# Kernel tuning notes

Hardware: AMD Instinct MI355X
Metric: run time of the kernel (lower is better)

Reference implementation:

```python
import jax, jax.numpy as jnp
import numpy as np

HDIM = 64

def setup_inputs() -> dict:
    key = jax.random.key(0)
    ks = jax.random.split(key, 5)
    B, T, D = 4, 2048, 1024
    x = jax.random.normal(ks[0], (B, T, D), dtype=jnp.float32)
    s = 1.0 / np.sqrt(D)
    W_qkv = jax.random.normal(ks[1], (D, 3 * D), dtype=jnp.float32) * s
    b_qkv = jax.random.normal(ks[2], (3 * D,), dtype=jnp.float32) * 0.02
    W_out = jax.random.normal(ks[3], (D, D), dtype=jnp.float32) * s
    b_out = jax.random.normal(ks[4], (D,), dtype=jnp.float32) * 0.02
    return {"x": x, "W_qkv": W_qkv, "b_qkv": b_qkv, "W_out": W_out, "b_out": b_out}

def reference(x, W_qkv, b_qkv, W_out, b_out):
    B, T, D = x.shape
    H = D // HDIM
    qkv = x @ W_qkv + b_qkv                          # [B,T,3D]
    q, k, v = jnp.split(qkv, 3, axis=-1)
    # [B,T,D] -> [B,H,T,Hdim]
    q = q.reshape(B, T, H, HDIM).transpose(0, 2, 1, 3)
    k = k.reshape(B, T, H, HDIM).transpose(0, 2, 1, 3)
    v = v.reshape(B, T, H, HDIM).transpose(0, 2, 1, 3)
    scores = jnp.einsum('bhqd,bhkd->bhqk', q, k) / jnp.sqrt(jnp.float32(HDIM))
    causal = jnp.tril(jnp.ones((T, T), dtype=bool))
    scores = jnp.where(causal[None, None], scores, -jnp.inf)
    weights = jax.nn.softmax(scores, axis=-1)        # dropout_prob=0 -> identity
    out = jnp.einsum('bhqk,bhkd->bhqd', weights, v)  # [B,H,T,Hdim]
    out = out.transpose(0, 2, 1, 3).reshape(B, T, D)
    return out @ W_out + b_out
```

## Files before the change

kernel.cpp:

```cpp
#include <hip/hip_runtime.h>

typedef __attribute__((ext_vector_type(8))) short short8;
typedef __attribute__((ext_vector_type(4))) short s16x4;
typedef __attribute__((ext_vector_type(4))) float f32x4;

#define AS1 __attribute__((address_space(1)))
#define AS3 __attribute__((address_space(3)))

__device__ __forceinline__ void gload_lds16(const void* g, void* l) {
  __builtin_amdgcn_global_load_lds((const AS1 void*)g, (AS3 void*)l, 16, 0, 0);
}

__device__ __forceinline__ unsigned short f2bf(float f) {
  unsigned int u = __float_as_uint(f);
  u += 0x7fffu + ((u >> 16) & 1u);
  return (unsigned short)(u >> 16);
}

__global__ __launch_bounds__(256) void k_convert(const float* __restrict__ in,
                                                 unsigned short* __restrict__ out) {
  long i = (long)blockIdx.x * 256 + threadIdx.x;
  const float4* p = (const float4*)in + i * 2;
  float4 a = p[0], b = p[1];
  short8 o;
  o[0] = (short)f2bf(a.x); o[1] = (short)f2bf(a.y);
  o[2] = (short)f2bf(a.z); o[3] = (short)f2bf(a.w);
  o[4] = (short)f2bf(b.x); o[5] = (short)f2bf(b.y);
  o[6] = (short)f2bf(b.z); o[7] = (short)f2bf(b.w);
  ((short8*)out)[i] = o;
}

__global__ __launch_bounds__(256) void k_transpose_w(const float* __restrict__ w,
                                                     unsigned short* __restrict__ wt,
                                                     int K, int N) {
  __shared__ float t[64][65];
  const int tilesN = N >> 6;
  const int tk = blockIdx.x / tilesN, tn = blockIdx.x % tilesN;
  const int c = threadIdx.x & 63, r0 = (threadIdx.x >> 6) * 16;
#pragma unroll
  for (int i = 0; i < 16; ++i)
    t[r0 + i][c] = w[(long)(tk * 64 + r0 + i) * N + tn * 64 + c];
  __syncthreads();
#pragma unroll
  for (int i = 0; i < 16; ++i)
    wt[(long)(tn * 64 + r0 + i) * K + tk * 64 + c] = f2bf(t[c][r0 + i]);
}

__global__ __launch_bounds__(256) void k_transpose_v(const unsigned short* __restrict__ qkv,
                                                     unsigned short* __restrict__ vt) {
  __shared__ __align__(16) unsigned short t[64][72];
  const int tt = blockIdx.x & 31, bh = blockIdx.x >> 5;
  const int b = bh >> 4, h = bh & 15;
  const int r = threadIdx.x >> 2, c0 = (threadIdx.x & 3) * 16;
  const unsigned short* src = qkv + (long)(b * 2048 + tt * 64 + r) * 3072 + 2048 + h * 64 + c0;
  *(short8*)&t[r][c0] = *(const short8*)src;
  *(short8*)&t[r][c0 + 8] = *(const short8*)(src + 8);
  __syncthreads();
  short8 w0, w1;
#pragma unroll
  for (int i = 0; i < 8; ++i) w0[i] = (short)t[c0 + i][r];
#pragma unroll
  for (int i = 0; i < 8; ++i) w1[i] = (short)t[c0 + 8 + i][r];
  unsigned short* dst = vt + (long)(bh * 64 + r) * 2048 + tt * 64 + c0;
  *(short8*)dst = w0;
  *(short8*)(dst + 8) = w1;
}

template <int OUT_BF16>
__global__ __launch_bounds__(256) void k_gemm(const unsigned short* __restrict__ A,
                                              const unsigned short* __restrict__ BT,
                                              const float* __restrict__ bias,
                                              void* __restrict__ out,
                                              int M, int N, int K) {
  __shared__ __align__(16) unsigned short As[2][128 * 64];
  __shared__ __align__(16) unsigned short Bs[2][128 * 64];
  const int tid = threadIdx.x, lane = tid & 63, wid = tid >> 6;
  const int r16 = lane & 15, khi = lane >> 4;
  const int wr = wid >> 1, wc = wid & 1;
  const int tilesN = N >> 7;
  const int cpx = gridDim.x >> 3;
  const int bid = ((int)blockIdx.x & 7) * cpx + ((int)blockIdx.x >> 3);
  const int tm = bid / tilesN, tn = bid % tilesN;
  const long m0 = (long)tm * 128, n0 = (long)tn * 128;
  f32x4 acc[4][4] = {};
  const int srow = tid >> 3;
  const int scol = ((tid & 7) ^ (srow & 7)) * 8;
  const unsigned short* aSrc = A + (m0 + srow) * K + scol;
  const unsigned short* bSrc = BT + (n0 + srow) * K + scol;
  unsigned short* aDst = &As[0][0] + tid * 8;
  unsigned short* bDst = &Bs[0][0] + tid * 8;
  const int nk = K >> 6;

#pragma unroll
  for (int call = 0; call < 4; ++call) {
    gload_lds16(aSrc + (long)call * 32 * K, aDst + call * 2048);
    gload_lds16(bSrc + (long)call * 32 * K, bDst + call * 2048);
  }

  int cur = 0;
  for (int ki = 0; ki < nk; ++ki) {
    __builtin_amdgcn_s_barrier();
    if (ki + 1 < nk) {
      const long k0 = (long)(ki + 1) * 64;
#pragma unroll
      for (int call = 0; call < 4; ++call) {
        gload_lds16(aSrc + (long)call * 32 * K + k0, aDst + (cur ^ 1) * 8192 + call * 2048);
        gload_lds16(bSrc + (long)call * 32 * K + k0, bDst + (cur ^ 1) * 8192 + call * 2048);
      }
      asm volatile("s_waitcnt vmcnt(8)" ::: "memory");
    } else {
      asm volatile("s_waitcnt vmcnt(0)" ::: "memory");
    }
    __builtin_amdgcn_s_barrier();
    __builtin_amdgcn_s_setprio(1);
#pragma unroll
    for (int kk = 0; kk < 2; ++kk) {
      const int pc = ((kk * 4 + khi) ^ (r16 & 7)) * 8;
      short8 af[4], bf[4];
#pragma unroll
      for (int m = 0; m < 4; ++m)
        af[m] = *(const short8*)&As[cur][(wr * 64 + m * 16 + r16) * 64 + pc];
#pragma unroll
      for (int n = 0; n < 4; ++n)
        bf[n] = *(const short8*)&Bs[cur][(wc * 64 + n * 16 + r16) * 64 + pc];
#pragma unroll
      for (int m = 0; m < 4; ++m)
#pragma unroll
        for (int n = 0; n < 4; ++n)
          acc[m][n] = __builtin_amdgcn_mfma_f32_16x16x32_bf16(af[m], bf[n], acc[m][n], 0, 0, 0);
    }
    __builtin_amdgcn_s_setprio(0);
    cur ^= 1;
  }
#pragma unroll
  for (int m = 0; m < 4; ++m) {
    long row = m0 + wr * 64 + m * 16 + khi * 4;
#pragma unroll
    for (int n = 0; n < 4; ++n) {
      int col = (int)n0 + wc * 64 + n * 16 + r16;
      float bv = bias[col];
#pragma unroll
      for (int j = 0; j < 4; ++j) {
        float v = acc[m][n][j] + bv;
        if (OUT_BF16)
          ((unsigned short*)out)[(row + j) * N + col] = f2bf(v);
        else
          ((float*)out)[(row + j) * N + col] = v;
      }
    }
  }
}

__global__ __launch_bounds__(512) void k_attn(const unsigned short* __restrict__ qkv,
                                              const unsigned short* __restrict__ vt,
                                              unsigned short* __restrict__ aout) {
  __shared__ __align__(16) unsigned short Ks[2][64 * 64];
  __shared__ __align__(16) unsigned short VTs[2][64 * 64];
  __shared__ __align__(16) unsigned short Ps[8][16 * 72];
  const int tid = threadIdx.x, lane = tid & 63, wid = tid >> 6;
  const int r16 = lane & 15, khi = lane >> 4;
  const int qt = 15 - (int)(blockIdx.x >> 6), bh = blockIdx.x & 63;
  const int b = bh >> 4, h = bh & 15;
  const long qrow0 = (long)b * 2048 + qt * 128;

  const int srow = wid * 8 + (lane >> 3);
  const int lck = (lane & 7) ^ (srow & 7);
  const unsigned short* kbase =
      qkv + ((long)b * 2048 + srow) * 3072 + 1024 + h * 64 + lck * 8;
  const unsigned short* vbase = vt + ((long)bh * 64 + srow) * 2048 + lck * 8;

  const long qrow = qrow0 + wid * 16 + r16;
  const short8 qf0 = *(const short8*)&qkv[qrow * 3072 + h * 64 + khi * 8];
  const short8 qf1 = *(const short8*)&qkv[qrow * 3072 + h * 64 + 32 + khi * 8];

  gload_lds16(kbase, &Ks[0][wid * 512]);
  gload_lds16(vbase, &VTs[0][wid * 512]);

  const int ktmax = 2 * qt + 1;
  const int ktw = (qt * 128 + wid * 16 + 15) >> 6;
  const int qg = qt * 128 + wid * 16 + r16;
  const float SC = 0.18033688f;
  float m_run = -1e30f, l_run = 0.f;
  f32x4 o[4] = {};

  for (int kt = 0; kt <= ktmax; ++kt) {
    const int cur = kt & 1;
    __builtin_amdgcn_s_barrier();
    if (kt < ktmax) {
      gload_lds16(kbase + (long)(kt + 1) * 64 * 3072, &Ks[cur ^ 1][wid * 512]);
      gload_lds16(vbase + (kt + 1) * 64, &VTs[cur ^ 1][wid * 512]);
      asm volatile("s_waitcnt vmcnt(2)" ::: "memory");
    } else {
      asm volatile("s_waitcnt vmcnt(0)" ::: "memory");
    }
    __builtin_amdgcn_s_barrier();
    if (kt > ktw) continue;

    f32x4 s[4] = {};
    __builtin_amdgcn_s_setprio(1);
#pragma unroll
    for (int kk = 0; kk < 2; ++kk) {
      const int pc = ((kk * 4 + khi) ^ (r16 & 7)) * 8;
      const short8 qf = kk ? qf1 : qf0;
#pragma unroll
      for (int n = 0; n < 4; ++n) {
        short8 kf = *(const short8*)&Ks[cur][(n * 16 + r16) * 64 + pc];
        s[n] = __builtin_amdgcn_mfma_f32_16x16x32_bf16(kf, qf, s[n], 0, 0, 0);
      }
    }
    __builtin_amdgcn_s_setprio(0);

    const bool need_mask = (kt * 64 + 63) > (qt * 128 + wid * 16);
    if (need_mask) {
      const int ktB = kt * 64;
#pragma unroll
      for (int n = 0; n < 4; ++n)
#pragma unroll
        for (int j = 0; j < 4; ++j)
          if ((ktB + n * 16 + khi * 4 + j) > qg) s[n][j] = -1e30f;
    }

    float pmn[4];
#pragma unroll
    for (int n = 0; n < 4; ++n)
      pmn[n] = fmaxf(fmaxf(s[n][0], s[n][1]), fmaxf(s[n][2], s[n][3]));
    float pm = fmaxf(fmaxf(pmn[0], pmn[1]), fmaxf(pmn[2], pmn[3]));
    pm = fmaxf(pm, __shfl_xor(pm, 16, 64));
    pm = fmaxf(pm, __shfl_xor(pm, 32, 64));
    const float pmS = pm * SC;
    const float mn = fmaxf(m_run, pmS);
    if (!__all(pmS <= m_run)) {
      const float alpha = __builtin_amdgcn_exp2f(m_run - mn);
      l_run *= alpha;
#pragma unroll
      for (int n = 0; n < 4; ++n)
#pragma unroll
        for (int j = 0; j < 4; ++j) o[n][j] *= alpha;
    }
    m_run = mn;

    const float nmn = -mn;
    float rsum = 0.f;
    unsigned int pk[8];
#pragma unroll
    for (int n = 0; n < 4; ++n) {
      float e0 = __builtin_amdgcn_exp2f(fmaf(s[n][0], SC, nmn));
      float e1 = __builtin_amdgcn_exp2f(fmaf(s[n][1], SC, nmn));
      float e2 = __builtin_amdgcn_exp2f(fmaf(s[n][2], SC, nmn));
      float e3 = __builtin_amdgcn_exp2f(fmaf(s[n][3], SC, nmn));
      rsum += (e0 + e1) + (e2 + e3);
      pk[n * 2] = __builtin_amdgcn_perm(__float_as_uint(e1), __float_as_uint(e0), 0x07060302u);
      pk[n * 2 + 1] = __builtin_amdgcn_perm(__float_as_uint(e3), __float_as_uint(e2), 0x07060302u);
    }
    rsum += __shfl_xor(rsum, 16, 64);
    rsum += __shfl_xor(rsum, 32, 64);
    l_run += rsum;

#pragma unroll
    for (int n = 0; n < 4; ++n) {
      uint2 pw = {pk[n * 2], pk[n * 2 + 1]};
      *(uint2*)&Ps[wid][r16 * 72 + n * 16 + khi * 4] = pw;
    }

    __builtin_amdgcn_s_setprio(1);
#pragma unroll
    for (int kk = 0; kk < 2; ++kk) {
      const short8 pf = *(const short8*)&Ps[wid][r16 * 72 + kk * 32 + khi * 8];
      const int pc = ((kk * 4 + khi) ^ (r16 & 7)) * 8;
#pragma unroll
      for (int n = 0; n < 4; ++n) {
        short8 vf = *(const short8*)&VTs[cur][(n * 16 + r16) * 64 + pc];
        o[n] = __builtin_amdgcn_mfma_f32_16x16x32_bf16(vf, pf, o[n], 0, 0, 0);
      }
    }
    __builtin_amdgcn_s_setprio(0);
  }

  const float inv = 1.f / l_run;
#pragma unroll
  for (int n = 0; n < 4; ++n) {
    s16x4 ow;
#pragma unroll
    for (int j = 0; j < 4; ++j) ow[j] = (short)f2bf(o[n][j] * inv);
    *(s16x4*)&aout[qrow * 1024 + h * 64 + n * 16 + khi * 4] = ow;
  }
}

extern "C" void kernel_launch(void* const* d_in, const int* in_sizes, int n_in,
                              void* d_out, int out_size, void* d_ws, size_t ws_size,
                              hipStream_t stream) {
  (void)in_sizes; (void)n_in; (void)out_size; (void)ws_size;
  const float* x = (const float*)d_in[0];
  const float* Wqkv = (const float*)d_in[1];
  const float* bqkv = (const float*)d_in[2];
  const float* Wout = (const float*)d_in[3];
  const float* bout = (const float*)d_in[4];
  char* ws = (char*)d_ws;
  unsigned short* xb    = (unsigned short*)(ws + 0);
  unsigned short* wqkvt = (unsigned short*)(ws + (16l << 20));
  unsigned short* woutt = (unsigned short*)(ws + (22l << 20));
  unsigned short* qkv   = (unsigned short*)(ws + (24l << 20));
  unsigned short* vt    = (unsigned short*)(ws + (72l << 20));
  unsigned short* aout  = xb;

  k_convert<<<4096, 256, 0, stream>>>(x, xb);
  k_transpose_w<<<768, 256, 0, stream>>>(Wqkv, wqkvt, 1024, 3072);
  k_transpose_w<<<256, 256, 0, stream>>>(Wout, woutt, 1024, 1024);
  k_gemm<1><<<64 * 24, 256, 0, stream>>>(xb, wqkvt, bqkv, qkv, 8192, 3072, 1024);
  k_transpose_v<<<2048, 256, 0, stream>>>(qkv, vt);
  k_attn<<<16 * 64, 512, 0, stream>>>(qkv, vt, aout);
  k_gemm<0><<<64 * 8, 256, 0, stream>>>(aout, woutt, bout, d_out, 8192, 1024, 1024);
}
```

Before: 247.9 us.

## Use 256x128 GEMM tiles with 8 waves and a 3-stage interleaved LDS pipeline

Grows the GEMM block tile to 256x128 with 512 threads and adds a triple-buffered LDS ring, prefetching two K-steps ahead. Global-to-LDS loads are split into chunks and interleaved between MFMA sub-phases, separated by barriers. The aim is better reuse of B tiles and more overlap of memory latency with MFMA work. In exchange it uses more LDS (144KB), adds extra barriers per K-step, and launches fewer blocks (256 for the output projection), which may leave CUs underused.

```diff
diff --git a/kernel.cpp b/kernel.cpp
--- a/kernel.cpp
+++ b/kernel.cpp
@@ -67,77 +67,107 @@
 }
 
 template <int OUT_BF16>
-__global__ __launch_bounds__(256) void k_gemm(const unsigned short* __restrict__ A,
+__global__ __launch_bounds__(512) void k_gemm(const unsigned short* __restrict__ A,
                                               const unsigned short* __restrict__ BT,
                                               const float* __restrict__ bias,
                                               void* __restrict__ out,
                                               int M, int N, int K) {
-  __shared__ __align__(16) unsigned short As[2][128 * 64];
-  __shared__ __align__(16) unsigned short Bs[2][128 * 64];
+  __shared__ __align__(16) unsigned short As[3][256 * 64];
+  __shared__ __align__(16) unsigned short Bs[3][128 * 64];
   const int tid = threadIdx.x, lane = tid & 63, wid = tid >> 6;
   const int r16 = lane & 15, khi = lane >> 4;
-  const int wr = wid >> 1, wc = wid & 1;
+  const int wm = wid >> 1, wn = wid & 1;
   const int tilesN = N >> 7;
   const int cpx = gridDim.x >> 3;
   const int bid = ((int)blockIdx.x & 7) * cpx + ((int)blockIdx.x >> 3);
   const int tm = bid / tilesN, tn = bid % tilesN;
-  const long m0 = (long)tm * 128, n0 = (long)tn * 128;
+  const long m0 = (long)tm * 256, n0 = (long)tn * 128;
   f32x4 acc[4][4] = {};
-  const int srow = tid >> 3;
-  const int scol = ((tid & 7) ^ (srow & 7)) * 8;
-  const unsigned short* aSrc = A + (m0 + srow) * K + scol;
-  const unsigned short* bSrc = BT + (n0 + srow) * K + scol;
-  unsigned short* aDst = &As[0][0] + tid * 8;
-  unsigned short* bDst = &Bs[0][0] + tid * 8;
+  const int lr8 = lane >> 3;
+  const int scol = ((lane & 7) ^ lr8) * 8;
+  const unsigned short* aSrc = A + (m0 + wid * 32 + lr8) * K + scol;
+  const unsigned short* bSrc = BT + (n0 + wid * 16 + lr8) * K + scol;
   const int nk = K >> 6;
-
-#pragma unroll
-  for (int call = 0; call < 4; ++call) {
-    gload_lds16(aSrc + (long)call * 32 * K, aDst + call * 2048);
-    gload_lds16(bSrc + (long)call * 32 * K, bDst + call * 2048);
+  const int pc0 = (khi ^ (r16 & 7)) * 8;
+  const int pc1 = ((4 + khi) ^ (r16 & 7)) * 8;
+
+#define SA(buf, kt, c) gload_lds16(aSrc + (long)(kt) * 64 + (c) * 8 * K, &As[buf][wid * 2048 + (c) * 512])
+#define SB(buf, kt, c) gload_lds16(bSrc + (long)(kt) * 64 + (c) * 8 * K, &Bs[buf][wid * 1024 + (c) * 512])
+#define AF(m, pc) (*(const short8*)&Ab[(wm * 64 + (m) * 16 + r16) * 64 + (pc)])
+#define BF(n, pc) (*(const short8*)&Bb[(wn * 64 + (n) * 16 + r16) * 64 + (pc)])
+
+  SA(0, 0, 0); SA(0, 0, 1); SA(0, 0, 2); SA(0, 0, 3); SB(0, 0, 0); SB(0, 0, 1);
+  if (nk > 1) { SA(1, 1, 0); SA(1, 1, 1); SA(1, 1, 2); SA(1, 1, 3); SB(1, 1, 0); SB(1, 1, 1); }
+
+  int ct = 0;
+  for (int t = 0; t < nk; ++t) {
+    const int st = (ct + 2 >= 3) ? ct - 1 : ct + 2;
+    if (t + 1 < nk) asm volatile("s_waitcnt vmcnt(6)" ::: "memory");
+    else            asm volatile("s_waitcnt vmcnt(0)" ::: "memory");
+    __builtin_amdgcn_s_barrier();
+    const bool stg = (t + 2) < nk;
+    const unsigned short* Ab = As[ct];
+    const unsigned short* Bb = Bs[ct];
+    short8 bf[4], af[2];
+
+    if (stg) { SA(st, t + 2, 0); SA(st, t + 2, 1); }
+    bf[0] = BF(0, pc0); bf[1] = BF(1, pc0); bf[2] = BF(2, pc0); bf[3] = BF(3, pc0);
+    af[0] = AF(0, pc0); af[1] = AF(1, pc0);
+    __builtin_amdgcn_s_setprio(1);
+#pragma unroll
+    for (int n = 0; n < 4; ++n) {
+      acc[0][n] = __builtin_amdgcn_mfma_f32_16x16x32_bf16(af[0], bf[n], acc[0][n], 0, 0, 0);
+      acc[1][n] = __builtin_amdgcn_mfma_f32_16x16x32_bf16(af[1], bf[n], acc[1][n], 0, 0, 0);
+    }
+    __builtin_amdgcn_s_setprio(0);
+    __builtin_amdgcn_s_barrier();
+
+    if (stg) { SA(st, t + 2, 2); SA(st, t + 2, 3); }
+    af[0] = AF(2, pc0); af[1] = AF(3, pc0);
+    __builtin_amdgcn_s_setprio(1);
+#pragma unroll
+    for (int n = 0; n < 4; ++n) {
+      acc[2][n] = __builtin_amdgcn_mfma_f32_16x16x32_bf16(af[0], bf[n], acc[2][n], 0, 0, 0);
+      acc[3][n] = __builtin_amdgcn_mfma_f32_16x16x32_bf16(af[1], bf[n], acc[3][n], 0, 0, 0);
+    }
+    __builtin_amdgcn_s_setprio(0);
+    __builtin_amdgcn_s_barrier();
+
+    if (stg) { SB(st, t + 2, 0); SB(st, t + 2, 1); }
+    bf[0] = BF(0, pc1); bf[1] = BF(1, pc1); bf[2] = BF(2, pc1); bf[3] = BF(3, pc1);
+    af[0] = AF(0, pc1); af[1] = AF(1, pc1);
+    __builtin_amdgcn_s_setprio(1);
+#pragma unroll
+    for (int n = 0; n < 4; ++n) {
+      acc[0][n] = __builtin_amdgcn_mfma_f32_16x16x32_bf16(af[0], bf[n], acc[0][n], 0, 0, 0);
+      acc[1][n] = __builtin_amdgcn_mfma_f32_16x16x32_bf16(af[1], bf[n], acc[1][n], 0, 0, 0);
+    }
+    __builtin_amdgcn_s_setprio(0);
+    __builtin_amdgcn_s_barrier();
+
+    af[0] = AF(2, pc1); af[1] = AF(3, pc1);
+    __builtin_amdgcn_s_setprio(1);
+#pragma unroll
+    for (int n = 0; n < 4; ++n) {
+      acc[2][n] = __builtin_amdgcn_mfma_f32_16x16x32_bf16(af[0], bf[n], acc[2][n], 0, 0, 0);
+      acc[3][n] = __builtin_amdgcn_mfma_f32_16x16x32_bf16(af[1], bf[n], acc[3][n], 0, 0, 0);
+    }
+    __builtin_amdgcn_s_setprio(0);
+    __builtin_amdgcn_s_barrier();
+
+    ct = (ct + 1 >= 3) ? 0 : ct + 1;
   }
-
-  int cur = 0;
-  for (int ki = 0; ki < nk; ++ki) {
-    __builtin_amdgcn_s_barrier();
-    if (ki + 1 < nk) {
-      const long k0 = (long)(ki + 1) * 64;
-#pragma unroll
-      for (int call = 0; call < 4; ++call) {
-        gload_lds16(aSrc + (long)call * 32 * K + k0, aDst + (cur ^ 1) * 8192 + call * 2048);
-        gload_lds16(bSrc + (long)call * 32 * K + k0, bDst + (cur ^ 1) * 8192 + call * 2048);
-      }
-      asm volatile("s_waitcnt vmcnt(8)" ::: "memory");
-    } else {
-      asm volatile("s_waitcnt vmcnt(0)" ::: "memory");
-    }
-    __builtin_amdgcn_s_barrier();
-    __builtin_amdgcn_s_setprio(1);
-#pragma unroll
-    for (int kk = 0; kk < 2; ++kk) {
-      const int pc = ((kk * 4 + khi) ^ (r16 & 7)) * 8;
-      short8 af[4], bf[4];
-#pragma unroll
-      for (int m = 0; m < 4; ++m)
-        af[m] = *(const short8*)&As[cur][(wr * 64 + m * 16 + r16) * 64 + pc];
-#pragma unroll
-      for (int n = 0; n < 4; ++n)
-        bf[n] = *(const short8*)&Bs[cur][(wc * 64 + n * 16 + r16) * 64 + pc];
-#pragma unroll
-      for (int m = 0; m < 4; ++m)
-#pragma unroll
-        for (int n = 0; n < 4; ++n)
-          acc[m][n] = __builtin_amdgcn_mfma_f32_16x16x32_bf16(af[m], bf[n], acc[m][n], 0, 0, 0);
-    }
-    __builtin_amdgcn_s_setprio(0);
-    cur ^= 1;
-  }
+#undef SA
+#undef SB
+#undef AF
+#undef BF
+
 #pragma unroll
   for (int m = 0; m < 4; ++m) {
-    long row = m0 + wr * 64 + m * 16 + khi * 4;
-#pragma unroll
-    for (int n = 0; n < 4; ++n) {
-      int col = (int)n0 + wc * 64 + n * 16 + r16;
+    long row = m0 + wm * 64 + m * 16 + khi * 4;
+#pragma unroll
+    for (int n = 0; n < 4; ++n) {
+      int col = (int)n0 + wn * 64 + n * 16 + r16;
       float bv = bias[col];
 #pragma unroll
       for (int j = 0; j < 4; ++j) {
@@ -306,8 +336,8 @@
   k_convert<<<4096, 256, 0, stream>>>(x, xb);
   k_transpose_w<<<768, 256, 0, stream>>>(Wqkv, wqkvt, 1024, 3072);
   k_transpose_w<<<256, 256, 0, stream>>>(Wout, woutt, 1024, 1024);
-  k_gemm<1><<<64 * 24, 256, 0, stream>>>(xb, wqkvt, bqkv, qkv, 8192, 3072, 1024);
+  k_gemm<1><<<32 * 24, 512, 0, stream>>>(xb, wqkvt, bqkv, qkv, 8192, 3072, 1024);
   k_transpose_v<<<2048, 256, 0, stream>>>(qkv, vt);
   k_attn<<<16 * 64, 512, 0, stream>>>(qkv, vt, aout);
-  k_gemm<0><<<64 * 8, 256, 0, stream>>>(aout, woutt, bout, d_out, 8192, 1024, 1024);
-}
+  k_gemm<0><<<32 * 8, 512, 0, stream>>>(aout, woutt, bout, d_out, 8192, 1024, 1024);
+}
```

Result: slower. 305.1 us (+23.1%).
